# Kernel tuning notes

Measured on AMD Instinct MI355X. Metric: run time of the kernel, lower is better.

The kernel has to match this reference:

```python
import jax, jax.numpy as jnp
import numpy as np
from jax import lax

PATCH = 8

def setup_inputs() -> dict:
    key = jax.random.key(0)
    ks = jax.random.split(key, 5)
    x = jax.random.normal(ks[0], (4, 64, 256, 256), dtype=jnp.float32)
    w_in = jax.random.normal(ks[1], (512, 64), dtype=jnp.float32) * 0.02
    b_in = jnp.zeros((512,), dtype=jnp.float32)
    w_dw = jax.random.normal(ks[2], (512, 1, 3, 3), dtype=jnp.float32) * 0.02
    b_dw = jnp.zeros((512,), dtype=jnp.float32)
    w_out = jax.random.normal(ks[3], (64, 256), dtype=jnp.float32) * 0.02
    b_out = jnp.zeros((64,), dtype=jnp.float32)
    fft_filter = jnp.ones((64, 1, 1, PATCH, PATCH // 2 + 1), dtype=jnp.float32)
    return {"x": x, "w_in": w_in, "b_in": b_in, "w_dw": w_dw, "b_dw": b_dw,
            "w_out": w_out, "b_out": b_out, "fft_filter": fft_filter}

def reference(x, w_in, b_in, w_dw, b_dw, w_out, b_out, fft_filter):
    # project_in: 1x1 conv == channel GEMM. x: [B, C, H, W] -> [B, 2h, H, W]
    h = jnp.einsum('oc,bchw->bohw', w_in, x) + b_in[None, :, None, None]
    # depthwise 3x3 conv, padding=1
    h = lax.conv_general_dilated(
        h, w_dw, window_strides=(1, 1), padding='SAME',
        dimension_numbers=('NCHW', 'OIHW', 'NCHW'),
        feature_group_count=w_dw.shape[0]) + b_dw[None, :, None, None]
    x1, x2 = jnp.split(h, 2, axis=1)
    h = jax.nn.gelu(x1, approximate=False) * x2  # exact GELU like F.gelu
    # project_out: 1x1 conv
    y = jnp.einsum('oc,bchw->bohw', w_out, h) + b_out[None, :, None, None]
    # patch-wise spectral filtering
    B, C, H, W = y.shape
    p = PATCH
    yp = y.reshape(B, C, H // p, p, W // p, p).transpose(0, 1, 2, 4, 3, 5)  # b c h w p1 p2
    yf = jnp.fft.rfft2(yp)              # b c h w p1 (p2//2+1)
    yf = yf * fft_filter                # filter broadcasts over (c,1,1,p1,p2r)
    yp = jnp.fft.irfft2(yf, s=(p, p))
    y = yp.transpose(0, 1, 2, 4, 3, 5).reshape(B, C, H, W)
    return y
```

## Files before the change

kernel.cpp:

```cpp
#include <hip/hip_runtime.h>
#include <math.h>

typedef __attribute__((ext_vector_type(8))) short short8;
typedef __attribute__((ext_vector_type(4))) float f32x4;
typedef __attribute__((ext_vector_type(2))) float f32x2;

#define TILE 16
#define IH 256
#define IW 256

#define WSA_OFF 16384
#define WSC_OFF 81920

#define H_STRIDE 1456
#define G_OFF 23296
#define SMEM_BYTES 39680

#define SP2(c) ((f32x2){(c), (c)})

__device__ __forceinline__ unsigned short f2bf(float f) {
  unsigned int u = __builtin_bit_cast(unsigned int, f);
  u = (u + 0x7FFFu + ((u >> 16) & 1u)) >> 16;
  return (unsigned short)u;
}

__global__ void edffn_prep(const float* __restrict__ fftf,
                           const float* __restrict__ w_in,
                           const float* __restrict__ w_out,
                           float* __restrict__ ws) {
  int blk = blockIdx.x, t = threadIdx.x;
  if (blk < 64) {
    int a = t >> 3, bb = t & 7;
    const float c0 = 0.70710678118654752f;
    const float ctab[8] = {1.f, c0, 0.f, -c0, -1.f, -c0, 0.f, c0};
    const float* F = fftf + blk * 40;
    float acc = 0.f;
    for (int k1 = 0; k1 < 8; ++k1)
      for (int k2 = 0; k2 < 8; ++k2) {
        float f = (k2 <= 4) ? F[k1 * 5 + k2] : F[((8 - k1) & 7) * 5 + (8 - k2)];
        acc += f * ctab[(k1 * a + k2 * bb) & 7];
      }
    ws[blk * 64 + t] = acc * (1.f / 64.f);
  } else if (blk < 128) {
    int b2 = blk - 64;
    int q = b2 >> 2, s = (b2 >> 1) & 1, ks = b2 & 1;
    int row = (s ? 256 : 0) + q * 16 + (t & 15);
    unsigned short* dst =
        (unsigned short*)((unsigned char*)ws + WSA_OFF) + (((q * 2 + s) * 2 + ks) * 64 + t) * 8;
    for (int j = 0; j < 8; ++j) {
      int k = ks * 32 + (t >> 4) * 8 + j;
      dst[j] = f2bf(w_in[row * 64 + k]);
    }
  } else {
    int b3 = blk - 128;
    int p = b3 >> 2, mt = b3 & 3;
    int row = mt * 16 + (t & 15);
    unsigned short* dst =
        (unsigned short*)((unsigned char*)ws + WSC_OFF) + ((p * 4 + mt) * 64 + t) * 8;
    for (int j = 0; j < 8; ++j) {
      int k = p * 32 + (t >> 4) * 8 + j;
      dst[j] = f2bf(w_out[row * 256 + k]);
    }
  }
}

__global__ __launch_bounds__(256, 2) void edffn_main(
    const float* __restrict__ x, const float* __restrict__ b_in,
    const float* __restrict__ w_dw, const float* __restrict__ b_dw,
    const float* __restrict__ b_out, const float* __restrict__ ws,
    float* __restrict__ out) {
  __shared__ __align__(16) unsigned char smem[SMEM_BYTES];
  __shared__ int s_flag;
  const int t = threadIdx.x;
  const int lane = t & 63, wave = t >> 6;
  const int l15 = lane & 15, lg = lane >> 4;
  const int gx0 = blockIdx.x * TILE, gy0 = blockIdx.y * TILE;
  const int b = blockIdx.z;
  const unsigned short* wsA = (const unsigned short*)((const unsigned char*)ws + WSA_OFF);
  const unsigned short* wsC = (const unsigned short*)((const unsigned char*)ws + WSC_OFF);

  short8 xf[6][2];
  int haddr[6];
  unsigned vmask = 0, imask = 0;
  const float* xb = x + (size_t)b * 64 * 65536;
#pragma unroll
  for (int i = 0; i < 6; ++i) {
    int nt = wave + 4 * i;
    int n = nt * 16 + l15;
    int hy = n / 18;
    int hx = n - hy * 18;
    int gy = gy0 + hy - 1, gx = gx0 + hx - 1;
    int vnt = (nt < 21) & (n < 324);
    int inb = vnt & (gy >= 0) & (gy < IH) & (gx >= 0) & (gx < IW);
    haddr[i] = hy * 80 + hx * 4;
    vmask |= (unsigned)vnt << i;
    imask |= (unsigned)inb << i;
    int gyc = min(max(gy, 0), IH - 1), gxc = min(max(gx, 0), IW - 1);
    const float* xp = xb + (size_t)gyc * IW + gxc;
#pragma unroll
    for (int ks = 0; ks < 2; ++ks) {
#pragma unroll
      for (int j = 0; j < 8; ++j) {
        int k = ks * 32 + lg * 8 + j;
        unsigned short bf = f2bf(xp[(size_t)k * 65536]);
        xf[i][ks][j] = (short)(inb ? bf : (unsigned short)0);
      }
    }
  }

  f32x4 accY[16];
#pragma unroll
  for (int i = 0; i < 16; ++i) accY[i] = (f32x4){0.f, 0.f, 0.f, 0.f};

  const int cp_dw = t & 15;
  const int oy_dw = t >> 4;

  auto loadWD = [&](int qq, unsigned (&wd)[9], unsigned& bd) {
    const int cg1 = qq * 16 + cp_dw, cg2 = 256 + qq * 16 + cp_dw;
#pragma unroll
    for (int u = 0; u < 9; ++u) {
      float w1 = w_dw[cg1 * 9 + u], w2 = w_dw[cg2 * 9 + u];
      asm("v_cvt_pkrtz_f16_f32 %0, %1, %2" : "=v"(wd[u]) : "v"(w1), "v"(w2));
    }
    float b1 = b_dw[cg1], b2 = b_dw[cg2];
    asm("v_cvt_pkrtz_f16_f32 %0, %1, %2" : "=v"(bd) : "v"(b1), "v"(b2));
  };

  unsigned wdC[9], wdN[9], bdC, bdN;
  short8 cfC;
  loadWD(0, wdC, bdC);
  cfC = *(const short8*)(wsC + ((0 * 4 + wave) * 64 + lane) * 8);

  for (int q = 0; q < 16; ++q) {
    {
      short8 af[2][2];
#pragma unroll
      for (int s = 0; s < 2; ++s)
#pragma unroll
        for (int ks = 0; ks < 2; ++ks)
          af[s][ks] = *(const short8*)(wsA + (((q * 2 + s) * 2 + ks) * 64 + lane) * 8);
      float bin[2][4];
#pragma unroll
      for (int s = 0; s < 2; ++s)
#pragma unroll
        for (int r = 0; r < 4; ++r) bin[s][r] = b_in[(s ? 256 : 0) + q * 16 + lg * 4 + r];
#pragma unroll
      for (int i = 0; i < 6; ++i) {
        if (wave + 4 * i < 21) {
          f32x4 acc0 = {0.f, 0.f, 0.f, 0.f}, acc1 = {0.f, 0.f, 0.f, 0.f};
          acc0 = __builtin_amdgcn_mfma_f32_16x16x32_bf16(af[0][0], xf[i][0], acc0, 0, 0, 0);
          acc0 = __builtin_amdgcn_mfma_f32_16x16x32_bf16(af[0][1], xf[i][1], acc0, 0, 0, 0);
          acc1 = __builtin_amdgcn_mfma_f32_16x16x32_bf16(af[1][0], xf[i][0], acc1, 0, 0, 0);
          acc1 = __builtin_amdgcn_mfma_f32_16x16x32_bf16(af[1][1], xf[i][1], acc1, 0, 0, 0);
          if ((vmask >> i) & 1u) {
            unsigned keep = (imask >> i) & 1u;
#pragma unroll
            for (int r = 0; r < 4; ++r) {
              float v0 = acc0[r] + bin[0][r];
              float v1 = acc1[r] + bin[1][r];
              unsigned pk;
              asm("v_cvt_pkrtz_f16_f32 %0, %1, %2" : "=v"(pk) : "v"(v0), "v"(v1));
              pk = keep ? pk : 0u;
              *(unsigned*)(smem + (lg * 4 + r) * H_STRIDE + haddr[i]) = pk;
            }
          }
        }
      }
    }
    if (q < 15) loadWD(q + 1, wdN, bdN);
    __syncthreads();

    {
      const int cp = cp_dw, oy = oy_dw;
      unsigned a[16];
#pragma unroll
      for (int j = 0; j < 16; ++j) a[j] = bdC;
#pragma unroll
      for (int dy = 0; dy < 3; ++dy) {
        const uint4* rp = (const uint4*)(smem + cp * H_STRIDE + (oy + dy) * 80);
        uint4 r0 = rp[0], r1 = rp[1], r2 = rp[2], r3 = rp[3];
        uint2 r4 = ((const uint2*)rp)[8];
        unsigned e[18] = {r0.x, r0.y, r0.z, r0.w, r1.x, r1.y, r1.z, r1.w,
                          r2.x, r2.y, r2.z, r2.w, r3.x, r3.y, r3.z, r3.w,
                          r4.x, r4.y};
#pragma unroll
        for (int ox = 0; ox < 16; ++ox) {
#pragma unroll
          for (int dx = 0; dx < 3; ++dx)
            asm("v_pk_fma_f16 %0, %1, %2, %0"
                : "+v"(a[ox])
                : "v"(wdC[dy * 3 + dx]), "v"(e[ox + dx]));
        }
      }
      const int c2 = (q & 1) * 16 + cp;
      const int gi = (c2 >> 3) ^ (oy & 3);
      unsigned short* Gp =
          (unsigned short*)(smem + G_OFF) + oy * 16 * 32 + gi * 8 + (c2 & 7);
#pragma unroll
      for (int j = 0; j < 8; ++j) {
        unsigned a0 = a[2 * j], a1 = a[2 * j + 1];
        unsigned a0h = a0 >> 16, a1h = a1 >> 16;
        f32x2 u, v;
        asm("v_cvt_f32_f16 %0, %1" : "=v"(u[0]) : "v"(a0));
        asm("v_cvt_f32_f16 %0, %1" : "=v"(u[1]) : "v"(a1));
        asm("v_cvt_f32_f16 %0, %1" : "=v"(v[0]) : "v"(a0h));
        asm("v_cvt_f32_f16 %0, %1" : "=v"(v[1]) : "v"(a1h));
        f32x2 z = u * 0.70710678118654752f;
        f32x2 z2 = z * z;
        f32x2 erfv;
        if (__builtin_expect(fmaxf(z2[0], z2[1]) > 0.16f, 0)) {
          erfv[0] = erff(z[0]);
          erfv[1] = erff(z[1]);
        } else {
          f32x2 p = __builtin_elementwise_fma(z2, SP2(1.f / 216.f), SP2(-1.f / 42.f));
          p = __builtin_elementwise_fma(z2, p, SP2(1.f / 10.f));
          p = __builtin_elementwise_fma(z2, p, SP2(-1.f / 3.f));
          p = __builtin_elementwise_fma(z2, p, SP2(1.f));
          erfv = 1.12837916709551257f * (z * p);
        }
        f32x2 tt = __builtin_elementwise_fma(erfv, SP2(0.5f), SP2(0.5f));
        f32x2 g = (u * tt) * v;
        Gp[(2 * j) * 32] = f2bf(g[0]);
        Gp[(2 * j + 1) * 32] = f2bf(g[1]);
      }
    }
    __syncthreads();

    if (q & 1) {
      const int p = q >> 1;
      const unsigned short* G = (const unsigned short*)(smem + G_OFF);
#pragma unroll
      for (int nt = 0; nt < 16; ++nt) {
        int g = lg ^ (nt & 3);
        int n = nt * 16 + l15;
        short8 bf = *(const short8*)(G + n * 32 + g * 8);
        accY[nt] = __builtin_amdgcn_mfma_f32_16x16x32_bf16(cfC, bf, accY[nt], 0, 0, 0);
      }
      if (q < 15)
        cfC = *(const short8*)(wsC + (((p + 1) * 4 + wave) * 64 + lane) * 8);
    }

    if (q < 15) {
#pragma unroll
      for (int u = 0; u < 9; ++u) wdC[u] = wdN[u];
      bdC = bdN;
    }
  }

  {
    f32x4 bo;
#pragma unroll
    for (int r = 0; r < 4; ++r) bo[r] = b_out[wave * 16 + lg * 4 + r];
#pragma unroll
    for (int nt = 0; nt < 16; ++nt)
#pragma unroll
      for (int r = 0; r < 4; ++r) accY[nt][r] += bo[r];
  }

  if (t == 0) s_flag = 1;
  __syncthreads();
  {
    int ok = 1;
    const float* kc = ws;
#pragma unroll
    for (int j = 0; j < 16; ++j) {
      int idx = t * 16 + j;
      float e = ((idx & 63) == 0) ? 1.f : 0.f;
      ok &= (fabsf(kc[idx] - e) <= 1e-5f) ? 1 : 0;
    }
    if (!ok) s_flag = 0;
  }
  __syncthreads();

  const int o = wave * 16 + lg * 4;
  if (s_flag) {
#pragma unroll
    for (int nt = 0; nt < 16; ++nt) {
      float* op = out + (((size_t)(b * 64 + o)) * IH + gy0 + nt) * IW + gx0 + l15;
#pragma unroll
      for (int r = 0; r < 4; ++r) op[(size_t)r * IH * IW] = accY[nt][r];
    }
    return;
  }

  float* YS = (float*)smem;
  for (int half = 0; half < 2; ++half) {
    __syncthreads();
    if ((wave >> 1) == half) {
      int c32 = (wave & 1) * 16 + lg * 4;
#pragma unroll
      for (int nt = 0; nt < 16; ++nt)
#pragma unroll
        for (int r = 0; r < 4; ++r) YS[(c32 + r) * 260 + nt * 16 + l15] = accY[nt][r];
    }
    __syncthreads();
    if (t < 128) {
      int o32 = t >> 2, oo = half * 32 + o32, qd = t & 3;
      const float* kp = ws + oo * 64;
      int py0 = (qd >> 1) * 8, px0 = (qd & 1) * 8;
      const float* row = YS + o32 * 260;
      for (int i = 0; i < 8; ++i)
        for (int j = 0; j < 8; ++j) {
          float acc = 0.f;
          for (int a_ = 0; a_ < 8; ++a_)
            for (int b_ = 0; b_ < 8; ++b_)
              acc += kp[a_ * 8 + b_] *
                     row[(py0 + ((i - a_) & 7)) * 16 + px0 + ((j - b_) & 7)];
          out[(((size_t)(b * 64 + oo)) * IH + gy0 + py0 + i) * IW + gx0 + px0 + j] = acc;
        }
    }
  }
}

extern "C" void kernel_launch(void* const* d_in, const int* in_sizes, int n_in,
                              void* d_out, int out_size, void* d_ws, size_t ws_size,
                              hipStream_t stream) {
  const float* x = (const float*)d_in[0];
  const float* w_in = (const float*)d_in[1];
  const float* b_in = (const float*)d_in[2];
  const float* w_dw = (const float*)d_in[3];
  const float* b_dw = (const float*)d_in[4];
  const float* w_out = (const float*)d_in[5];
  const float* b_out = (const float*)d_in[6];
  const float* fftf = (const float*)d_in[7];
  float* out = (float*)d_out;
  float* ws = (float*)d_ws;

  edffn_prep<<<160, 64, 0, stream>>>(fftf, w_in, w_out, ws);
  dim3 grid(IW / TILE, IH / TILE, 4);
  edffn_main<<<grid, 256, 0, stream>>>(x, b_in, w_dw, b_dw, b_out, ws, out);
}
```

Measured before the change: 156.4 us.

## Double-buffer gated tile and compute GELU in packed fp16 with fp16 MFMA

```diff
diff --git a/kernel.cpp b/kernel.cpp
--- a/kernel.cpp
+++ b/kernel.cpp
@@ -4,6 +4,7 @@
 typedef __attribute__((ext_vector_type(8))) short short8;
 typedef __attribute__((ext_vector_type(4))) float f32x4;
 typedef __attribute__((ext_vector_type(2))) float f32x2;
+typedef _Float16 f16x8 __attribute__((ext_vector_type(8)));
 
 #define TILE 16
 #define IH 256
@@ -14,9 +15,8 @@
 
 #define H_STRIDE 1456
 #define G_OFF 23296
-#define SMEM_BYTES 39680
-
-#define SP2(c) ((f32x2){(c), (c)})
+#define G_BUF 16384
+#define SMEM_BYTES 56064
 
 __device__ __forceinline__ unsigned short f2bf(float f) {
   unsigned int u = __builtin_bit_cast(unsigned int, f);
@@ -59,7 +59,8 @@
         (unsigned short*)((unsigned char*)ws + WSC_OFF) + ((p * 4 + mt) * 64 + t) * 8;
     for (int j = 0; j < 8; ++j) {
       int k = p * 32 + (t >> 4) * 8 + j;
-      dst[j] = f2bf(w_out[row * 256 + k]);
+      _Float16 hv = (_Float16)w_out[row * 256 + k];
+      dst[j] = __builtin_bit_cast(unsigned short, hv);
     }
   }
 }
@@ -126,10 +127,26 @@
     asm("v_cvt_pkrtz_f16_f32 %0, %1, %2" : "=v"(bd) : "v"(b1), "v"(b2));
   };
 
+#define PKC(nm, val)                                                        \
+  unsigned nm;                                                              \
+  {                                                                         \
+    float fv = (val);                                                       \
+    asm("v_cvt_pkrtz_f16_f32 %0, %1, %1" : "=v"(nm) : "v"(fv));             \
+  }
+  PKC(kSQ, 0.70710678f)
+  PKC(kC216, 1.f / 216.f)
+  PKC(kCm42, -1.f / 42.f)
+  PKC(kC10, 0.1f)
+  PKC(kCm3, -1.f / 3.f)
+  PKC(kOne, 1.0f)
+  PKC(kHalf, 0.5f)
+  PKC(kErf, 1.12837917f)
+#undef PKC
+
   unsigned wdC[9], wdN[9], bdC, bdN;
-  short8 cfC;
+  f16x8 cfC;
   loadWD(0, wdC, bdC);
-  cfC = *(const short8*)(wsC + ((0 * 4 + wave) * 64 + lane) * 8);
+  cfC = *(const f16x8*)(wsC + ((0 * 4 + wave) * 64 + lane) * 8);
 
   for (int q = 0; q < 16; ++q) {
     {
@@ -170,6 +187,20 @@
     if (q < 15) loadWD(q + 1, wdN, bdN);
     __syncthreads();
 
+    if (q >= 2 && !(q & 1)) {
+      const int pc = (q >> 1) - 1;
+      const unsigned short* G =
+          (const unsigned short*)(smem + G_OFF + (pc & 1) * G_BUF);
+#pragma unroll
+      for (int nt = 0; nt < 16; ++nt) {
+        int g = lg ^ (nt & 3);
+        int n = nt * 16 + l15;
+        f16x8 bf = *(const f16x8*)(G + n * 32 + g * 8);
+        accY[nt] = __builtin_amdgcn_mfma_f32_16x16x32_f16(cfC, bf, accY[nt], 0, 0, 0);
+      }
+      cfC = *(const f16x8*)(wsC + (((pc + 1) * 4 + wave) * 64 + lane) * 8);
+    }
+
     {
       const int cp = cp_dw, oy = oy_dw;
       unsigned a[16];
@@ -194,56 +225,77 @@
       }
       const int c2 = (q & 1) * 16 + cp;
       const int gi = (c2 >> 3) ^ (oy & 3);
-      unsigned short* Gp =
-          (unsigned short*)(smem + G_OFF) + oy * 16 * 32 + gi * 8 + (c2 & 7);
+      unsigned short* Gp = (unsigned short*)(smem + G_OFF + ((q >> 1) & 1) * G_BUF) +
+                           oy * 16 * 32 + gi * 8 + (c2 & 7);
+      unsigned umax = 0;
+      unsigned gw[8];
 #pragma unroll
       for (int j = 0; j < 8; ++j) {
         unsigned a0 = a[2 * j], a1 = a[2 * j + 1];
-        unsigned a0h = a0 >> 16, a1h = a1 >> 16;
-        f32x2 u, v;
-        asm("v_cvt_f32_f16 %0, %1" : "=v"(u[0]) : "v"(a0));
-        asm("v_cvt_f32_f16 %0, %1" : "=v"(u[1]) : "v"(a1));
-        asm("v_cvt_f32_f16 %0, %1" : "=v"(v[0]) : "v"(a0h));
-        asm("v_cvt_f32_f16 %0, %1" : "=v"(v[1]) : "v"(a1h));
-        f32x2 z = u * 0.70710678118654752f;
-        f32x2 z2 = z * z;
-        f32x2 erfv;
-        if (__builtin_expect(fmaxf(z2[0], z2[1]) > 0.16f, 0)) {
-          erfv[0] = erff(z[0]);
-          erfv[1] = erff(z[1]);
-        } else {
-          f32x2 p = __builtin_elementwise_fma(z2, SP2(1.f / 216.f), SP2(-1.f / 42.f));
-          p = __builtin_elementwise_fma(z2, p, SP2(1.f / 10.f));
-          p = __builtin_elementwise_fma(z2, p, SP2(-1.f / 3.f));
-          p = __builtin_elementwise_fma(z2, p, SP2(1.f));
-          erfv = 1.12837916709551257f * (z * p);
+        unsigned u = __builtin_amdgcn_perm(a1, a0, 0x05040100u);
+        unsigned v = __builtin_amdgcn_perm(a1, a0, 0x07060302u);
+        unsigned uabs = u & 0x7FFF7FFFu;
+        asm("v_pk_max_f16 %0, %1, %2" : "=v"(umax) : "v"(umax), "v"(uabs));
+        unsigned z, z2, p, erfv, tt, g;
+        asm("v_pk_mul_f16 %0, %1, %2" : "=v"(z) : "v"(u), "v"(kSQ));
+        asm("v_pk_mul_f16 %0, %1, %2" : "=v"(z2) : "v"(z), "v"(z));
+        asm("v_pk_fma_f16 %0, %1, %2, %3" : "=v"(p) : "v"(z2), "v"(kC216), "v"(kCm42));
+        asm("v_pk_fma_f16 %0, %1, %2, %3" : "=v"(p) : "v"(z2), "v"(p), "v"(kC10));
+        asm("v_pk_fma_f16 %0, %1, %2, %3" : "=v"(p) : "v"(z2), "v"(p), "v"(kCm3));
+        asm("v_pk_fma_f16 %0, %1, %2, %3" : "=v"(p) : "v"(z2), "v"(p), "v"(kOne));
+        asm("v_pk_mul_f16 %0, %1, %2" : "=v"(erfv) : "v"(z), "v"(p));
+        asm("v_pk_mul_f16 %0, %1, %2" : "=v"(erfv) : "v"(erfv), "v"(kErf));
+        asm("v_pk_fma_f16 %0, %1, %2, %2" : "=v"(tt) : "v"(erfv), "v"(kHalf));
+        asm("v_pk_mul_f16 %0, %1, %2" : "=v"(g) : "v"(u), "v"(tt));
+        asm("v_pk_mul_f16 %0, %1, %2" : "=v"(g) : "v"(g), "v"(v));
+        gw[j] = g;
+      }
+      {
+        float m0, m1;
+        unsigned uh = umax >> 16;
+        asm("v_cvt_f32_f16 %0, %1" : "=v"(m0) : "v"(umax));
+        asm("v_cvt_f32_f16 %0, %1" : "=v"(m1) : "v"(uh));
+        if (__builtin_expect(fmaxf(m0, m1) > 0.565685f, 0)) {
+#pragma unroll
+          for (int j = 0; j < 8; ++j) {
+            float g01[2];
+#pragma unroll
+            for (int kx = 0; kx < 2; ++kx) {
+              unsigned aw = a[2 * j + kx], ah = aw >> 16;
+              float hu, hv2;
+              asm("v_cvt_f32_f16 %0, %1" : "=v"(hu) : "v"(aw));
+              asm("v_cvt_f32_f16 %0, %1" : "=v"(hv2) : "v"(ah));
+              g01[kx] = 0.5f * hu * (1.f + erff(hu * 0.70710678f)) * hv2;
+            }
+            unsigned pk;
+            asm("v_cvt_pkrtz_f16_f32 %0, %1, %2" : "=v"(pk) : "v"(g01[0]), "v"(g01[1]));
+            gw[j] = pk;
+          }
         }
-        f32x2 tt = __builtin_elementwise_fma(erfv, SP2(0.5f), SP2(0.5f));
-        f32x2 g = (u * tt) * v;
-        Gp[(2 * j) * 32] = f2bf(g[0]);
-        Gp[(2 * j + 1) * 32] = f2bf(g[1]);
+      }
+#pragma unroll
+      for (int j = 0; j < 8; ++j) {
+        Gp[(2 * j) * 32] = (unsigned short)gw[j];
+        Gp[(2 * j + 1) * 32] = (unsigned short)(gw[j] >> 16);
       }
     }
     __syncthreads();
-
-    if (q & 1) {
-      const int p = q >> 1;
-      const unsigned short* G = (const unsigned short*)(smem + G_OFF);
-#pragma unroll
-      for (int nt = 0; nt < 16; ++nt) {
-        int g = lg ^ (nt & 3);
-        int n = nt * 16 + l15;
-        short8 bf = *(const short8*)(G + n * 32 + g * 8);
-        accY[nt] = __builtin_amdgcn_mfma_f32_16x16x32_bf16(cfC, bf, accY[nt], 0, 0, 0);
-      }
-      if (q < 15)
-        cfC = *(const short8*)(wsC + (((p + 1) * 4 + wave) * 64 + lane) * 8);
-    }
 
     if (q < 15) {
 #pragma unroll
       for (int u = 0; u < 9; ++u) wdC[u] = wdN[u];
       bdC = bdN;
+    }
+  }
+
+  {
+    const unsigned short* G = (const unsigned short*)(smem + G_OFF + G_BUF);
+#pragma unroll
+    for (int nt = 0; nt < 16; ++nt) {
+      int g = lg ^ (nt & 3);
+      int n = nt * 16 + l15;
+      f16x8 bf = *(const f16x8*)(G + n * 32 + g * 8);
+      accY[nt] = __builtin_amdgcn_mfma_f32_16x16x32_f16(cfC, bf, accY[nt], 0, 0, 0);
     }
   }
 
```

Measured after the change: 150.2 us. 4.0% less time.
